# Kernel optimization log

Hardware: AMD Instinct MI355X
Metric: run time of the kernel (lower is better)

## Reference

```python
import jax, jax.numpy as jnp
import numpy as np

IN_DIM, HID, N_EXP, TOP_K = 4096, 512, 128, 2
SMOOTH = 0.1
SPARSITY = 0.5

def _gelu(x):
    return jax.nn.gelu(x, approximate=False)  # torch nn.GELU default (erf)


def setup_inputs() -> dict:
    key = jax.random.key(0)
    ks = jax.random.split(key, 24)
    def lin(k, fan_in, shape):
        bound = 1.0 / np.sqrt(fan_in)
        return jax.random.uniform(k, shape, jnp.float32, -bound, bound)
    x = jax.random.normal(ks[0], (4, 2048, IN_DIM), jnp.float32)
    # weights stored as (in, out); apply with x @ W + b
    w_in_proj = lin(ks[1], IN_DIM, (IN_DIM, HID)); b_in_proj = lin(ks[2], IN_DIM, (HID,))
    w_ff1 = lin(ks[3], 2 * HID, (2 * HID, HID)); b_ff1 = lin(ks[4], 2 * HID, (HID,))
    w_ff2 = lin(ks[5], HID, (HID, HID)); b_ff2 = lin(ks[6], HID, (HID,))
    w_ta = lin(ks[7], HID, (HID, HID)); b_ta = lin(ks[8], HID, (HID,))
    w_tb = lin(ks[9], HID, (HID, HID)); b_tb = lin(ks[10], HID, (HID,))
    w_iw = lin(ks[11], HID, (HID, HID)); b_iw = lin(ks[12], HID, (HID,))
    input_b = jnp.zeros((HID,), jnp.float32)
    mask = (jax.random.uniform(ks[13], (HID, HID)) > SPARSITY).astype(jnp.float32)
    w_rw = lin(ks[14], HID, (HID, HID)) * mask  # structured sparsity on recurrent weight
    r_b = jnp.zeros((HID,), jnp.float32)
    w_g1 = lin(ks[15], HID, (HID, 2 * HID)); b_g1 = lin(ks[16], HID, (2 * HID,))
    w_g2 = lin(ks[17], 2 * HID, (2 * HID, N_EXP)); b_g2 = lin(ks[18], 2 * HID, (N_EXP,))
    return dict(x=x, w_in_proj=w_in_proj, b_in_proj=b_in_proj, w_ff1=w_ff1, b_ff1=b_ff1,
                w_ff2=w_ff2, b_ff2=b_ff2, w_ta=w_ta, b_ta=b_ta, w_tb=w_tb, b_tb=b_tb,
                w_iw=w_iw, b_iw=b_iw, input_b=input_b, w_rw=w_rw, r_b=r_b,
                w_g1=w_g1, b_g1=b_g1, w_g2=w_g2, b_g2=b_g2)


def reference(x, w_in_proj, b_in_proj, w_ff1, b_ff1, w_ff2, b_ff2, w_ta, b_ta,
              w_tb, b_tb, w_iw, b_iw, input_b, w_rw, r_b, w_g1, b_g1, w_g2, b_g2):
    B, S, _ = x.shape
    ts = 1.0

    def step(carry, x_t):
        h, prev_probs, first = carry
        xt = x_t @ w_in_proj + b_in_proj                       # (B, HID)
        # CfC cell
        x_cat = jnp.concatenate([xt, h], axis=-1)
        ff1 = _gelu(x_cat @ w_ff1 + b_ff1)
        ff2 = _gelu(ff1 @ w_ff2 + b_ff2)
        t_a = ff2 @ w_ta + b_ta
        t_b = ff2 @ w_tb + b_tb
        t_interp = jax.nn.sigmoid(t_a * ts + t_b)
        inp_c = _gelu(xt @ w_iw + b_iw + input_b)
        rec_c = _gelu(h @ w_rw + r_b)
        new_h = h * (1.0 - t_interp) + t_interp * (inp_c + rec_c)
        # expert gate
        g = _gelu(new_h @ w_g1 + b_g1)
        probs = jax.nn.softmax(g @ w_g2 + b_g2, axis=-1)       # (B, N_EXP)
        probs = jnp.where(first, probs,
                          (1.0 - SMOOTH) * probs + SMOOTH * prev_probs)
        new_prev = jax.lax.stop_gradient(probs)                # .detach() in torch
        top_p, top_i = jax.lax.top_k(probs, TOP_K)
        top_w = top_p / jnp.sum(top_p, axis=-1, keepdims=True)
        return (new_h, new_prev, jnp.array(False)), (top_i, top_w)

    h0 = jnp.zeros((B, HID), x.dtype)
    p0 = jnp.zeros((B, N_EXP), x.dtype)
    carry0 = (h0, p0, jnp.array(True))
    _, (idx, wts) = jax.lax.scan(step, carry0, jnp.swapaxes(x, 0, 1))
    expert_indices = jnp.swapaxes(idx, 0, 1)   # (B, S, TOP_K)
    expert_weights = jnp.swapaxes(wts, 0, 1)   # (B, S, TOP_K)
    return expert_indices, expert_weights
```

## Files before the change

kernel.cpp:

```cpp
#include <hip/hip_runtime.h>
#include <cmath>

#define HID 512
#define NEXP 128
#define BB 4
#define SS 2048
#define NROW (BB*SS)
#define FAST_ITERS 96
#define FAIL_STICKY 12

typedef unsigned long long u64;
typedef unsigned int u32;

__device__ __forceinline__ float gelu_f(float x){
  return 0.5f*x*(1.0f + erff(x*0.70710678118654752440f));
}

__device__ __forceinline__ u64 aload64(const u64* p){
  return __hip_atomic_load(p, __ATOMIC_RELAXED, __HIP_MEMORY_SCOPE_AGENT);
}
__device__ __forceinline__ void astore64(u64* p, u64 v){
  __hip_atomic_store(p, v, __ATOMIC_RELAXED, __HIP_MEMORY_SCOPE_AGENT);
}
__device__ __forceinline__ void fstore64(u64* p, u64 v){
  asm volatile("global_store_dwordx2 %0, %1, off" :: "v"(p), "v"(v) : "memory");
}
__device__ __forceinline__ u64 packtag(float f, u32 tag){
  return ((u64)__float_as_uint(f) << 32) | (u64)tag;
}

__device__ __forceinline__ void poll2x(const u64* fb, const u64* mb, u32 tag,
                                       float* stg, int tid,
                                       int& fails, bool& use_agent){
  u64 v0 = 0, v1 = 0;
  bool ok0 = false, ok1 = false;
  if (!use_agent){
    const u64* p0 = fb + tid;
    const u64* p1 = fb + tid + 256;
    for (int it = 0; it < FAST_ITERS; ++it){
      u64 a, b;
      asm volatile("global_load_dwordx2 %0, %2, off sc0\n\t"
                   "global_load_dwordx2 %1, %3, off sc0\n\t"
                   "s_waitcnt vmcnt(0)"
                   : "=&v"(a), "=&v"(b) : "v"(p0), "v"(p1) : "memory");
      if (!ok0 && (u32)a == tag){ ok0 = true; v0 = a; }
      if (!ok1 && (u32)b == tag){ ok1 = true; v1 = b; }
      if (ok0 && ok1) break;
    }
    if (!(ok0 && ok1)){
      if (++fails >= FAIL_STICKY) use_agent = true;
    }
  }
  if (!ok0){ const u64* q = mb + tid;       u64 a; do { a = aload64(q); } while ((u32)a != tag); v0 = a; }
  if (!ok1){ const u64* q = mb + tid + 256; u64 a; do { a = aload64(q); } while ((u32)a != tag); v1 = a; }
  stg[tid]       = __uint_as_float((u32)(v0 >> 32));
  stg[tid + 256] = __uint_as_float((u32)(v1 >> 32));
}

__global__ __launch_bounds__(256) void biwc_k(const float* __restrict__ b_iw,
                                              const float* __restrict__ input_b,
                                              float* __restrict__ biwc)
{
  int i = blockIdx.x*256 + threadIdx.x;
  if (i < HID) biwc[i] = b_iw[i] + input_b[i];
}

template<bool GELU>
__global__ __launch_bounds__(256) void gemm_k(
    const float* __restrict__ A, const float* __restrict__ W,
    const float* __restrict__ bias, float* __restrict__ C,
    int M, int N, int K)
{
  __shared__ float As[16][68];
  __shared__ float Ws[16][68];
  const int tid = threadIdx.x;
  const int mb = blockIdx.y*64, nb = blockIdx.x*64;
  const int tx = tid & 15, ty = tid >> 4;
  const int am = tid >> 2, ak = (tid & 3)*4;
  const int wk = tid >> 4, wn = (tid & 15)*4;
  float acc[4][4] = {};
  const float* Aptr = A + (size_t)(mb+am)*K + ak;
  for (int kt = 0; kt < K; kt += 16){
    float4 av = *(const float4*)(Aptr + kt);
    float4 wv = *(const float4*)(W + (size_t)(kt+wk)*N + nb + wn);
    As[ak  ][am] = av.x; As[ak+1][am] = av.y; As[ak+2][am] = av.z; As[ak+3][am] = av.w;
    *(float4*)&Ws[wk][wn] = wv;
    __syncthreads();
#pragma unroll
    for (int kk = 0; kk < 16; kk++){
      float4 a4 = *(const float4*)&As[kk][ty*4];
      float4 w4 = *(const float4*)&Ws[kk][tx*4];
      float ar[4] = {a4.x, a4.y, a4.z, a4.w};
      float wr[4] = {w4.x, w4.y, w4.z, w4.w};
#pragma unroll
      for (int i = 0; i < 4; i++)
#pragma unroll
        for (int j = 0; j < 4; j++)
          acc[i][j] = fmaf(ar[i], wr[j], acc[i][j]);
    }
    __syncthreads();
  }
#pragma unroll
  for (int i = 0; i < 4; i++){
    int row = mb + ty*4 + i;
    float o[4];
#pragma unroll
    for (int j = 0; j < 4; j++){
      float v = acc[i][j] + bias[nb + tx*4 + j];
      o[j] = GELU ? gelu_f(v) : v;
    }
    float4 o4 = {o[0], o[1], o[2], o[3]};
    *(float4*)(C + (size_t)row*N + nb + tx*4) = o4;
  }
}

__global__ __launch_bounds__(256, 1) void scan_k(
    const float* __restrict__ w_ff1, const float* __restrict__ w_rw,
    const float* __restrict__ w_ff2,
    const float* __restrict__ w_ta, const float* __restrict__ w_tb,
    const float* __restrict__ bff2, const float* __restrict__ b_ta,
    const float* __restrict__ b_tb, const float* __restrict__ rb,
    const float* __restrict__ PRE, const float* __restrict__ INPC,
    float* __restrict__ Hout,
    u64* __restrict__ exh, u64* __restrict__ exf1, u64* __restrict__ exf2,
    u64* __restrict__ fexh, u64* __restrict__ fexf1, u64* __restrict__ fexf2)
{
  __shared__ float Wa2[512*32];
  __shared__ float Wb2[512*16];
  __shared__ float Wc2[512*16];
  __shared__ float stg[512];
  __shared__ float red[128];
  __shared__ float rec_loc[16];

  const int tid = threadIdx.x;
  const int b = blockIdx.x & 7;
  if (b >= BB) return;
  const int sub = blockIdx.x >> 3;
  const int col0 = sub*16;
  u64* exh_b   = exh   + b*512;
  u64* exf1_b  = exf1  + b*512;
  u64* exf2_b  = exf2  + b*512;
  u64* fexh_b  = fexh  + b*512;
  u64* fexf1_b = fexf1 + b*512;
  u64* fexf2_b = fexf2 + b*512;

  if (tid < 16) fstore64(&fexh_b[col0 + tid], packtag(0.f, 0u));

  for (int idx = tid; idx < 512*32; idx += 256){
    int k = idx >> 5, c = idx & 31;
    float v = (c < 16) ? w_ff1[(size_t)(512+k)*HID + col0 + c]
                       : w_rw[(size_t)k*HID + col0 + (c-16)];
    Wa2[((k>>1)<<6) + (c<<1) + (k&1)] = v;
  }
  for (int idx = tid; idx < 512*16; idx += 256){
    int k = idx >> 4, c = idx & 15;
    Wb2[((k>>1)<<5) + (c<<1) + (k&1)] = w_ff2[(size_t)k*HID + col0 + c];
    Wc2[((k>>1)<<5) + (c<<1) + (k&1)] = w_ta[(size_t)k*HID + col0 + c]
                                      + w_tb[(size_t)k*HID + col0 + c];
  }
  float b3v = 0.f, bff2v = 0.f, rbv = 0.f, h_reg = 0.f;
  if (tid < 16){ b3v = b_ta[col0+tid] + b_tb[col0+tid]; bff2v = bff2[col0+tid]; }
  if (tid >= 16 && tid < 32) rbv = rb[col0 + tid - 16];
  __syncthreads();

  const int cA = tid & 31, pA = tid >> 5;
  const int cB = tid & 15, pB = tid >> 4;
  int fails = 0; bool use_agent = false;

  for (int t = 0; t < SS; t++){
    float pre_v = 0.f, ic_v = 0.f;
    if (tid < 16){
      pre_v = PRE [((size_t)b*SS + t)*HID + col0 + tid];
      ic_v  = INPC[((size_t)b*SS + t)*HID + col0 + tid];
    }
    poll2x(fexh_b, exh_b, (u32)t, stg, tid, fails, use_agent);
    __syncthreads();
    {
      const float2* wp = (const float2*)(Wa2) + (pA<<5) + cA;
      const float2* hp = (const float2*)(stg) + pA;
      float a0=0.f, a1=0.f, a2=0.f, a3=0.f;
#pragma unroll
      for (int j = 0; j < 32; j += 2){
        float2 w0 = wp[(j+0)*256], h0 = hp[(j+0)*8];
        float2 w1 = wp[(j+1)*256], h1 = hp[(j+1)*8];
        a0 = fmaf(w0.x, h0.x, a0); a1 = fmaf(w0.y, h0.y, a1);
        a2 = fmaf(w1.x, h1.x, a2); a3 = fmaf(w1.y, h1.y, a3);
      }
      float acc = (a0+a1)+(a2+a3);
      acc += __shfl_xor(acc, 32);
      if ((tid & 32) == 0) red[(tid>>6)*32 + cA] = acc;
    }
    __syncthreads();
    if (tid < 32){
      float s = red[tid] + red[32+tid] + red[64+tid] + red[96+tid];
      if (tid < 16){
        float v = gelu_f(pre_v + s);
        u64 pk = packtag(v, (u32)(t+1));
        fstore64(&fexf1_b[col0 + tid], pk);
        astore64(&exf1_b[col0 + tid], pk);
      } else {
        rec_loc[tid-16] = gelu_f(s + rbv);
      }
    }
    poll2x(fexf1_b, exf1_b, (u32)(t+1), stg, tid, fails, use_agent);
    __syncthreads();
    {
      const float2* wp = (const float2*)(Wb2) + (pB<<4) + cB;
      const float2* hp = (const float2*)(stg) + pB;
      float a0=0.f, a1=0.f, a2=0.f, a3=0.f;
#pragma unroll
      for (int j = 0; j < 16; j += 2){
        float2 w0 = wp[(j+0)*256], h0 = hp[(j+0)*16];
        float2 w1 = wp[(j+1)*256], h1 = hp[(j+1)*16];
        a0 = fmaf(w0.x, h0.x, a0); a1 = fmaf(w0.y, h0.y, a1);
        a2 = fmaf(w1.x, h1.x, a2); a3 = fmaf(w1.y, h1.y, a3);
      }
      float acc = (a0+a1)+(a2+a3);
      acc += __shfl_xor(acc, 16);
      acc += __shfl_xor(acc, 32);
      if ((tid & 48) == 0) red[(tid>>6)*16 + cB] = acc;
    }
    __syncthreads();
    if (tid < 16){
      float s = red[tid] + red[16+tid] + red[32+tid] + red[48+tid];
      float v = gelu_f(s + bff2v);
      u64 pk = packtag(v, (u32)(t+1));
      fstore64(&fexf2_b[col0 + tid], pk);
      astore64(&exf2_b[col0 + tid], pk);
    }
    poll2x(fexf2_b, exf2_b, (u32)(t+1), stg, tid, fails, use_agent);
    __syncthreads();
    {
      const float2* wp = (const float2*)(Wc2) + (pB<<4) + cB;
      const float2* hp = (const float2*)(stg) + pB;
      float a0=0.f, a1=0.f, a2=0.f, a3=0.f;
#pragma unroll
      for (int j = 0; j < 16; j += 2){
        float2 w0 = wp[(j+0)*256], h0 = hp[(j+0)*16];
        float2 w1 = wp[(j+1)*256], h1 = hp[(j+1)*16];
        a0 = fmaf(w0.x, h0.x, a0); a1 = fmaf(w0.y, h0.y, a1);
        a2 = fmaf(w1.x, h1.x, a2); a3 = fmaf(w1.y, h1.y, a3);
      }
      float acc = (a0+a1)+(a2+a3);
      acc += __shfl_xor(acc, 16);
      acc += __shfl_xor(acc, 32);
      if ((tid & 48) == 0) red[(tid>>6)*16 + cB] = acc;
    }
    __syncthreads();
    if (tid < 16){
      float s = red[tid] + red[16+tid] + red[32+tid] + red[48+tid];
      float ti = 1.0f / (1.0f + expf(-(s + b3v)));
      float nh = h_reg*(1.0f - ti) + ti*(ic_v + rec_loc[tid]);
      h_reg = nh;
      u64 pk = packtag(nh, (u32)(t+1));
      fstore64(&fexh_b[col0 + tid], pk);
      astore64(&exh_b[col0 + tid], pk);
      Hout[((size_t)b*SS + t)*HID + col0 + tid] = nh;
    }
  }

  __syncthreads();
  for (int i = tid; i < 512; i += 256){
    fstore64(&fexh_b[i],  0xFFFFFFFFull);
    fstore64(&fexf1_b[i], 0xFFFFFFFFull);
    fstore64(&fexf2_b[i], 0xFFFFFFFFull);
  }
}

__global__ __launch_bounds__(256) void softmax_k(const float* __restrict__ LOGITS,
                                                 float* __restrict__ SM)
{
  int wv = threadIdx.x >> 6, lane = threadIdx.x & 63;
  int row = blockIdx.x*4 + wv;
  const float* xp = LOGITS + (size_t)row*NEXP;
  float x0 = xp[lane], x1 = xp[lane+64];
  float m = fmaxf(x0, x1);
#pragma unroll
  for (int d = 1; d < 64; d <<= 1) m = fmaxf(m, __shfl_xor(m, d));
  float e0 = expf(x0 - m), e1 = expf(x1 - m);
  float s = e0 + e1;
#pragma unroll
  for (int d = 1; d < 64; d <<= 1) s += __shfl_xor(s, d);
  float inv = 1.0f / s;
  float* op = SM + (size_t)row*NEXP;
  op[lane] = e0*inv; op[lane+64] = e1*inv;
}

__global__ __launch_bounds__(256) void smooth_topk_k(const float* __restrict__ SM,
                                                     float* __restrict__ out)
{
  int wv = threadIdx.x >> 6, lane = threadIdx.x & 63;
  int row = blockIdx.x*4 + wv;
  int b = row >> 11, t = row & 2047;
  const float* base = SM + (size_t)row*NEXP;
  float a0 = 0.f, a1 = 0.f;
  float coef = 0.9f;
  int nt = t < 20 ? t : 20;
  for (int j = 0; j < nt; j++){
    const float* pj = base - j*NEXP;
    a0 += coef * pj[lane];
    a1 += coef * pj[lane+64];
    coef *= 0.1f;
  }
  if (t < 20){
    const float* s0 = SM + (size_t)b*SS*NEXP;
    float c0 = coef * (1.0f/0.9f);
    a0 += c0 * s0[lane];
    a1 += c0 * s0[lane+64];
  }
  float v0, v1; int i0, i1;
  if (a0 >= a1){ v0=a0; i0=lane;    v1=a1; i1=lane+64; }
  else         { v0=a1; i0=lane+64; v1=a0; i1=lane;    }
#pragma unroll
  for (int d = 1; d < 64; d <<= 1){
    float ov0 = __shfl_xor(v0, d), ov1 = __shfl_xor(v1, d);
    int   oi0 = __shfl_xor(i0, d), oi1 = __shfl_xor(i1, d);
    bool firstMine = (v0 > ov0) || (v0 == ov0 && i0 < oi0);
    float nv0, nv1; int ni0, ni1;
    if (firstMine){
      nv0 = v0; ni0 = i0;
      bool s = (v1 > ov0) || (v1 == ov0 && i1 < oi0);
      nv1 = s ? v1 : ov0; ni1 = s ? i1 : oi0;
    } else {
      nv0 = ov0; ni0 = oi0;
      bool s = (ov1 > v0) || (ov1 == v0 && oi1 < i0);
      nv1 = s ? ov1 : v0; ni1 = s ? oi1 : i0;
    }
    v0 = nv0; v1 = nv1; i0 = ni0; i1 = ni1;
  }
  if (lane == 0){
    float ssum = v0 + v1;
    size_t o = (size_t)row*2;
    out[o]     = (float)i0;
    out[o+1]   = (float)i1;
    out[16384 + o]   = v0 / ssum;
    out[16384 + o+1] = v1 / ssum;
  }
}

extern "C" void kernel_launch(void* const* d_in, const int* in_sizes, int n_in,
                              void* d_out, int out_size, void* d_ws, size_t ws_size,
                              hipStream_t stream)
{
  (void)in_sizes; (void)n_in; (void)out_size;
  const float* x       = (const float*)d_in[0];
  const float* w_in    = (const float*)d_in[1];
  const float* b_in    = (const float*)d_in[2];
  const float* w_ff1   = (const float*)d_in[3];
  const float* b_ff1   = (const float*)d_in[4];
  const float* w_ff2   = (const float*)d_in[5];
  const float* b_ff2   = (const float*)d_in[6];
  const float* w_ta    = (const float*)d_in[7];
  const float* b_ta    = (const float*)d_in[8];
  const float* w_tb    = (const float*)d_in[9];
  const float* b_tb    = (const float*)d_in[10];
  const float* w_iw    = (const float*)d_in[11];
  const float* b_iw    = (const float*)d_in[12];
  const float* input_b = (const float*)d_in[13];
  const float* w_rw    = (const float*)d_in[14];
  const float* r_b     = (const float*)d_in[15];
  const float* w_g1    = (const float*)d_in[16];
  const float* b_g1    = (const float*)d_in[17];
  const float* w_g2    = (const float*)d_in[18];
  const float* b_g2    = (const float*)d_in[19];

  float* ws    = (float*)d_ws;
  float* XT    = ws + 0;
  float* PRE   = ws + 4194304;
  float* INPC  = ws + 8388608;
  float* Hbuf  = ws + 12582912;
  float* G1    = ws + 0;
  float* LOGB  = ws + 8388608;
  float* SM    = ws + 9437184;
  float* biwc  = ws + 16777216;
  u64*   exh   = (u64*)(ws + 16777728);
  u64*   exf1  = (u64*)(ws + 16781824);
  u64*   exf2  = (u64*)(ws + 16785920);
  u64*   fexh  = (u64*)(ws + 16790016);
  u64*   fexf1 = (u64*)(ws + 16794112);
  u64*   fexf2 = (u64*)(ws + 16798208);
  if (ws_size < (size_t)16802304 * sizeof(float)) return;

  hipMemsetAsync(ws + 16777728, 0, 3 * 2048 * sizeof(u64), stream);

  biwc_k<<<2, 256, 0, stream>>>(b_iw, input_b, biwc);
  gemm_k<false><<<dim3(8, 128), 256, 0, stream>>>(x, w_in, b_in, XT, NROW, 512, 4096);
  gemm_k<false><<<dim3(8, 128), 256, 0, stream>>>(XT, w_ff1, b_ff1, PRE, NROW, 512, 512);
  gemm_k<true ><<<dim3(8, 128), 256, 0, stream>>>(XT, w_iw, biwc, INPC, NROW, 512, 512);
  scan_k<<<256, 256, 0, stream>>>(w_ff1, w_rw, w_ff2, w_ta, w_tb,
                                  b_ff2, b_ta, b_tb, r_b,
                                  PRE, INPC, Hbuf, exh, exf1, exf2,
                                  fexh, fexf1, fexf2);
  gemm_k<true ><<<dim3(16, 128), 256, 0, stream>>>(Hbuf, w_g1, b_g1, G1, NROW, 1024, 512);
  gemm_k<false><<<dim3(2, 128), 256, 0, stream>>>(G1, w_g2, b_g2, LOGB, NROW, 128, 1024);
  softmax_k<<<2048, 256, 0, stream>>>(LOGB, SM);
  smooth_topk_k<<<2048, 256, 0, stream>>>(SM, (float*)d_out);
}
```

Measured before the change: 11.00 ms.

## Keep recurrent weights in registers and reduce via wave shuffles, drop block barriers

```diff
diff --git a/kernel.cpp b/kernel.cpp
--- a/kernel.cpp
+++ b/kernel.cpp
@@ -29,8 +29,8 @@
   return ((u64)__float_as_uint(f) << 32) | (u64)tag;
 }
 
-__device__ __forceinline__ void poll2x(const u64* fb, const u64* mb, u32 tag,
-                                       float* stg, int tid,
+__device__ __forceinline__ void poll2p(const u64* fb, const u64* mb, u32 tag,
+                                       float* stgp, int tid,
                                        int& fails, bool& use_agent){
   u64 v0 = 0, v1 = 0;
   bool ok0 = false, ok1 = false;
@@ -53,8 +53,9 @@
   }
   if (!ok0){ const u64* q = mb + tid;       u64 a; do { a = aload64(q); } while ((u32)a != tag); v0 = a; }
   if (!ok1){ const u64* q = mb + tid + 256; u64 a; do { a = aload64(q); } while ((u32)a != tag); v1 = a; }
-  stg[tid]       = __uint_as_float((u32)(v0 >> 32));
-  stg[tid + 256] = __uint_as_float((u32)(v1 >> 32));
+  int k0 = tid, k1 = tid + 256;
+  stgp[k0 + 4*(k0>>6)] = __uint_as_float((u32)(v0 >> 32));
+  stgp[k1 + 4*(k1>>6)] = __uint_as_float((u32)(v1 >> 32));
 }
 
 __global__ __launch_bounds__(256) void biwc_k(const float* __restrict__ b_iw,
@@ -125,11 +126,11 @@
     u64* __restrict__ exh, u64* __restrict__ exf1, u64* __restrict__ exf2,
     u64* __restrict__ fexh, u64* __restrict__ fexf1, u64* __restrict__ fexf2)
 {
-  __shared__ float Wa2[512*32];
-  __shared__ float Wb2[512*16];
-  __shared__ float Wc2[512*16];
-  __shared__ float stg[512];
-  __shared__ float red[128];
+  __shared__ float stg_h[544];
+  __shared__ float stg_f1[544];
+  __shared__ float stg_f2[544];
+  __shared__ float pre_buf[64*16];
+  __shared__ float ic_buf[64*16];
   __shared__ float rec_loc[16];
 
   const int tid = threadIdx.x;
@@ -144,121 +145,139 @@
   u64* fexf1_b = fexf1 + b*512;
   u64* fexf2_b = fexf2 + b*512;
 
-  if (tid < 16) fstore64(&fexh_b[col0 + tid], packtag(0.f, 0u));
-
-  for (int idx = tid; idx < 512*32; idx += 256){
-    int k = idx >> 5, c = idx & 31;
-    float v = (c < 16) ? w_ff1[(size_t)(512+k)*HID + col0 + c]
-                       : w_rw[(size_t)k*HID + col0 + (c-16)];
-    Wa2[((k>>1)<<6) + (c<<1) + (k&1)] = v;
-  }
-  for (int idx = tid; idx < 512*16; idx += 256){
-    int k = idx >> 4, c = idx & 15;
-    Wb2[((k>>1)<<5) + (c<<1) + (k&1)] = w_ff2[(size_t)k*HID + col0 + c];
-    Wc2[((k>>1)<<5) + (c<<1) + (k&1)] = w_ta[(size_t)k*HID + col0 + c]
-                                      + w_tb[(size_t)k*HID + col0 + c];
-  }
-  float b3v = 0.f, bff2v = 0.f, rbv = 0.f, h_reg = 0.f;
-  if (tid < 16){ b3v = b_ta[col0+tid] + b_tb[col0+tid]; bff2v = bff2[col0+tid]; }
-  if (tid >= 16 && tid < 32) rbv = rb[col0 + tid - 16];
-  __syncthreads();
-
-  const int cA = tid & 31, pA = tid >> 5;
-  const int cB = tid & 15, pB = tid >> 4;
+  const int w = tid >> 6, l = tid & 63;
+  const int outA = w*8 + (l & 7), kpA = l >> 3;
+  const int outB = w*4 + (l & 3), kpB = l >> 2;
+
+  if (l < 4) fstore64(&fexh_b[col0 + outB], packtag(0.f, 0u));
+
+  float wA[64], wB[32], wC[32];
+  {
+    const float* srcA = (outA < 16)
+        ? (w_ff1 + (size_t)(512 + kpA*64)*HID + col0 + outA)
+        : (w_rw  + (size_t)(kpA*64)*HID + col0 + outA - 16);
+#pragma unroll
+    for (int j = 0; j < 64; j++) wA[j] = srcA[(size_t)j*HID];
+    const float* srcB  = w_ff2 + (size_t)(kpB*32)*HID + col0 + outB;
+    const float* srcC1 = w_ta  + (size_t)(kpB*32)*HID + col0 + outB;
+    const float* srcC2 = w_tb  + (size_t)(kpB*32)*HID + col0 + outB;
+#pragma unroll
+    for (int j = 0; j < 32; j++){
+      wB[j] = srcB[(size_t)j*HID];
+      wC[j] = srcC1[(size_t)j*HID] + srcC2[(size_t)j*HID];
+    }
+  }
+  const float rbv   = (outA >= 16) ? rb[col0 + outA - 16] : 0.f;
+  const float bff2v = bff2[col0 + outB];
+  const float b3v   = b_ta[col0 + outB] + b_tb[col0 + outB];
+  float h_reg = 0.f;
+
+  const int baseA = kpA*68;
+  const int baseB = kpB*32 + 4*(kpB >> 1);
+
   int fails = 0; bool use_agent = false;
 
   for (int t = 0; t < SS; t++){
-    float pre_v = 0.f, ic_v = 0.f;
-    if (tid < 16){
-      pre_v = PRE [((size_t)b*SS + t)*HID + col0 + tid];
-      ic_v  = INPC[((size_t)b*SS + t)*HID + col0 + tid];
-    }
-    poll2x(fexh_b, exh_b, (u32)t, stg, tid, fails, use_agent);
+    if ((t & 63) == 0){
+      __syncthreads();
+      int s = tid >> 2, j4 = (tid & 3) << 2;
+      float4 pv = *(const float4*)(PRE  + ((size_t)b*SS + t + s)*HID + col0 + j4);
+      float4 qv = *(const float4*)(INPC + ((size_t)b*SS + t + s)*HID + col0 + j4);
+      *(float4*)&pre_buf[s*16 + j4] = pv;
+      *(float4*)&ic_buf [s*16 + j4] = qv;
+    }
+    poll2p(fexh_b, exh_b, (u32)t, stg_h, tid, fails, use_agent);
     __syncthreads();
     {
-      const float2* wp = (const float2*)(Wa2) + (pA<<5) + cA;
-      const float2* hp = (const float2*)(stg) + pA;
+      const float* hp = &stg_h[baseA];
       float a0=0.f, a1=0.f, a2=0.f, a3=0.f;
 #pragma unroll
-      for (int j = 0; j < 32; j += 2){
-        float2 w0 = wp[(j+0)*256], h0 = hp[(j+0)*8];
-        float2 w1 = wp[(j+1)*256], h1 = hp[(j+1)*8];
-        a0 = fmaf(w0.x, h0.x, a0); a1 = fmaf(w0.y, h0.y, a1);
-        a2 = fmaf(w1.x, h1.x, a2); a3 = fmaf(w1.y, h1.y, a3);
+      for (int j = 0; j < 16; j++){
+        float4 h4 = *(const float4*)(hp + j*4);
+        a0 = fmaf(h4.x, wA[j*4+0], a0);
+        a1 = fmaf(h4.y, wA[j*4+1], a1);
+        a2 = fmaf(h4.z, wA[j*4+2], a2);
+        a3 = fmaf(h4.w, wA[j*4+3], a3);
       }
       float acc = (a0+a1)+(a2+a3);
+      acc += __shfl_xor(acc, 8);
+      acc += __shfl_xor(acc, 16);
       acc += __shfl_xor(acc, 32);
-      if ((tid & 32) == 0) red[(tid>>6)*32 + cA] = acc;
-    }
-    __syncthreads();
-    if (tid < 32){
-      float s = red[tid] + red[32+tid] + red[64+tid] + red[96+tid];
-      if (tid < 16){
-        float v = gelu_f(pre_v + s);
-        u64 pk = packtag(v, (u32)(t+1));
-        fstore64(&fexf1_b[col0 + tid], pk);
-        astore64(&exf1_b[col0 + tid], pk);
-      } else {
-        rec_loc[tid-16] = gelu_f(s + rbv);
-      }
-    }
-    poll2x(fexf1_b, exf1_b, (u32)(t+1), stg, tid, fails, use_agent);
+      if (l < 8){
+        if (outA < 16){
+          float v = gelu_f(pre_buf[(t & 63)*16 + outA] + acc);
+          u64 pk = packtag(v, (u32)(t+1));
+          fstore64(&fexf1_b[col0 + outA], pk);
+          astore64(&exf1_b[col0 + outA], pk);
+        } else {
+          rec_loc[outA - 16] = gelu_f(acc + rbv);
+        }
+      }
+    }
+    poll2p(fexf1_b, exf1_b, (u32)(t+1), stg_f1, tid, fails, use_agent);
     __syncthreads();
     {
-      const float2* wp = (const float2*)(Wb2) + (pB<<4) + cB;
-      const float2* hp = (const float2*)(stg) + pB;
+      const float* fp = &stg_f1[baseB];
       float a0=0.f, a1=0.f, a2=0.f, a3=0.f;
 #pragma unroll
-      for (int j = 0; j < 16; j += 2){
-        float2 w0 = wp[(j+0)*256], h0 = hp[(j+0)*16];
-        float2 w1 = wp[(j+1)*256], h1 = hp[(j+1)*16];
-        a0 = fmaf(w0.x, h0.x, a0); a1 = fmaf(w0.y, h0.y, a1);
-        a2 = fmaf(w1.x, h1.x, a2); a3 = fmaf(w1.y, h1.y, a3);
+      for (int j = 0; j < 8; j++){
+        float4 f4 = *(const float4*)(fp + j*4);
+        a0 = fmaf(f4.x, wB[j*4+0], a0);
+        a1 = fmaf(f4.y, wB[j*4+1], a1);
+        a2 = fmaf(f4.z, wB[j*4+2], a2);
+        a3 = fmaf(f4.w, wB[j*4+3], a3);
       }
       float acc = (a0+a1)+(a2+a3);
+      acc += __shfl_xor(acc, 4);
+      acc += __shfl_xor(acc, 8);
       acc += __shfl_xor(acc, 16);
       acc += __shfl_xor(acc, 32);
-      if ((tid & 48) == 0) red[(tid>>6)*16 + cB] = acc;
-    }
-    __syncthreads();
-    if (tid < 16){
-      float s = red[tid] + red[16+tid] + red[32+tid] + red[48+tid];
-      float v = gelu_f(s + bff2v);
-      u64 pk = packtag(v, (u32)(t+1));
-      fstore64(&fexf2_b[col0 + tid], pk);
-      astore64(&exf2_b[col0 + tid], pk);
-    }
-    poll2x(fexf2_b, exf2_b, (u32)(t+1), stg, tid, fails, use_agent);
+      if (l < 4){
+        float v = gelu_f(acc + bff2v);
+        u64 pk = packtag(v, (u32)(t+1));
+        fstore64(&fexf2_b[col0 + outB], pk);
+        astore64(&exf2_b[col0 + outB], pk);
+      }
+    }
+    poll2p(fexf2_b, exf2_b, (u32)(t+1), stg_f2, tid, fails, use_agent);
     __syncthreads();
     {
-      const float2* wp = (const float2*)(Wc2) + (pB<<4) + cB;
-      const float2* hp = (const float2*)(stg) + pB;
+      const float* fp = &stg_f2[baseB];
       float a0=0.f, a1=0.f, a2=0.f, a3=0.f;
 #pragma unroll
-      for (int j = 0; j < 16; j += 2){
-        float2 w0 = wp[(j+0)*256], h0 = hp[(j+0)*16];
-        float2 w1 = wp[(j+1)*256], h1 = hp[(j+1)*16];
-        a0 = fmaf(w0.x, h0.x, a0); a1 = fmaf(w0.y, h0.y, a1);
-        a2 = fmaf(w1.x, h1.x, a2); a3 = fmaf(w1.y, h1.y, a3);
+      for (int j = 0; j < 8; j++){
+        float4 f4 = *(const float4*)(fp + j*4);
+        a0 = fmaf(f4.x, wC[j*4+0], a0);
+        a1 = fmaf(f4.y, wC[j*4+1], a1);
+        a2 = fmaf(f4.z, wC[j*4+2], a2);
+        a3 = fmaf(f4.w, wC[j*4+3], a3);
       }
       float acc = (a0+a1)+(a2+a3);
+      acc += __shfl_xor(acc, 4);
+      acc += __shfl_xor(acc, 8);
       acc += __shfl_xor(acc, 16);
       acc += __shfl_xor(acc, 32);
-      if ((tid & 48) == 0) red[(tid>>6)*16 + cB] = acc;
-    }
-    __syncthreads();
-    if (tid < 16){
-      float s = red[tid] + red[16+tid] + red[32+tid] + red[48+tid];
-      float ti = 1.0f / (1.0f + expf(-(s + b3v)));
-      float nh = h_reg*(1.0f - ti) + ti*(ic_v + rec_loc[tid]);
+      float ti = 1.0f / (1.0f + expf(-(acc + b3v)));
+      float rc = rec_loc[outB];
+      float ic = ic_buf[(t & 63)*16 + outB];
+      float nh = h_reg*(1.0f - ti) + ti*(ic + rc);
       h_reg = nh;
-      u64 pk = packtag(nh, (u32)(t+1));
-      fstore64(&fexh_b[col0 + tid], pk);
-      astore64(&exh_b[col0 + tid], pk);
-      Hout[((size_t)b*SS + t)*HID + col0 + tid] = nh;
-    }
-  }
-
+      if (l < 4){
+        u64 pk = packtag(nh, (u32)(t+1));
+        fstore64(&fexh_b[col0 + outB], pk);
+        astore64(&exh_b[col0 + outB], pk);
+        Hout[((size_t)b*SS + t)*HID + col0 + outB] = nh;
+      }
+    }
+  }
+
+  {
+    const u64* q0 = exh_b + tid;
+    const u64* q1 = exh_b + tid + 256;
+    u64 a;
+    do { a = aload64(q0); } while ((u32)a != (u32)SS);
+    do { a = aload64(q1); } while ((u32)a != (u32)SS);
+  }
   __syncthreads();
   for (int i = tid; i < 512; i += 256){
     fstore64(&fexh_b[i],  0xFFFFFFFFull);
```

New measurement: 13.67 ms. 24.3% more time.

## Bind scan chains to XCDs via hardware XCC ID and dynamic slot claiming

Applied to the files above, without the earlier changes.

```diff
diff --git a/kernel.cpp b/kernel.cpp
--- a/kernel.cpp
+++ b/kernel.cpp
@@ -7,7 +7,8 @@
 #define SS 2048
 #define NROW (BB*SS)
 #define FAST_ITERS 96
-#define FAIL_STICKY 12
+#define FAIL_STICKY 16
+#define WARMUP_T 16
 
 typedef unsigned long long u64;
 typedef unsigned int u32;
@@ -22,6 +23,9 @@
 __device__ __forceinline__ void astore64(u64* p, u64 v){
   __hip_atomic_store(p, v, __ATOMIC_RELAXED, __HIP_MEMORY_SCOPE_AGENT);
 }
+__device__ __forceinline__ int aloadi(const int* p){
+  return __hip_atomic_load(p, __ATOMIC_RELAXED, __HIP_MEMORY_SCOPE_AGENT);
+}
 __device__ __forceinline__ void fstore64(u64* p, u64 v){
   asm volatile("global_store_dwordx2 %0, %1, off" :: "v"(p), "v"(v) : "memory");
 }
@@ -31,7 +35,7 @@
 
 __device__ __forceinline__ void poll2x(const u64* fb, const u64* mb, u32 tag,
                                        float* stg, int tid,
-                                       int& fails, bool& use_agent){
+                                       int& fails, bool& use_agent, bool count){
   u64 v0 = 0, v1 = 0;
   bool ok0 = false, ok1 = false;
   if (!use_agent){
@@ -47,7 +51,7 @@
       if (!ok1 && (u32)b == tag){ ok1 = true; v1 = b; }
       if (ok0 && ok1) break;
     }
-    if (!(ok0 && ok1)){
+    if (!(ok0 && ok1) && count){
       if (++fails >= FAIL_STICKY) use_agent = true;
     }
   }
@@ -123,7 +127,8 @@
     const float* __restrict__ PRE, const float* __restrict__ INPC,
     float* __restrict__ Hout,
     u64* __restrict__ exh, u64* __restrict__ exf1, u64* __restrict__ exf2,
-    u64* __restrict__ fexh, u64* __restrict__ fexf1, u64* __restrict__ fexf2)
+    u64* __restrict__ fexh, u64* __restrict__ fexf1, u64* __restrict__ fexf2,
+    int* __restrict__ ctl)
 {
   __shared__ float Wa2[512*32];
   __shared__ float Wb2[512*16];
@@ -131,12 +136,40 @@
   __shared__ float stg[512];
   __shared__ float red[128];
   __shared__ float rec_loc[16];
+  __shared__ int sh_chain, sh_sub;
 
   const int tid = threadIdx.x;
-  const int b = blockIdx.x & 7;
-  if (b >= BB) return;
-  const int sub = blockIdx.x >> 3;
+
+  if (tid == 0){
+    u32 xcc;
+    asm volatile("s_getreg_b32 %0, hwreg(HW_REG_XCC_ID)" : "=s"(xcc));
+    int xcd = (int)(xcc & 7);
+    int chain = -1, sub = -1;
+    if (xcd < BB){
+      int s = __hip_atomic_fetch_add(&ctl[xcd], 1, __ATOMIC_RELAXED, __HIP_MEMORY_SCOPE_AGENT);
+      if (s < 32){ chain = xcd; sub = s;
+        __hip_atomic_fetch_add(&ctl[4], 1, __ATOMIC_RELAXED, __HIP_MEMORY_SCOPE_AGENT); }
+    }
+    if (chain < 0){
+      for (int spin = 0; spin < 8000; ++spin){
+        if (aloadi(&ctl[4]) >= BB*32) break;
+        __builtin_amdgcn_s_sleep(2);
+      }
+      if (aloadi(&ctl[4]) < BB*32){
+        for (int c = 0; c < BB && chain < 0; c++){
+          int s = __hip_atomic_fetch_add(&ctl[c], 1, __ATOMIC_RELAXED, __HIP_MEMORY_SCOPE_AGENT);
+          if (s < 32){ chain = c; sub = s;
+            __hip_atomic_fetch_add(&ctl[4], 1, __ATOMIC_RELAXED, __HIP_MEMORY_SCOPE_AGENT); }
+        }
+      }
+    }
+    sh_chain = chain; sh_sub = sub;
+  }
+  __syncthreads();
+  const int b = sh_chain, sub = sh_sub;
+  if (b < 0) return;
   const int col0 = sub*16;
+
   u64* exh_b   = exh   + b*512;
   u64* exf1_b  = exf1  + b*512;
   u64* exf2_b  = exf2  + b*512;
@@ -163,17 +196,25 @@
   if (tid >= 16 && tid < 32) rbv = rb[col0 + tid - 16];
   __syncthreads();
 
+  if (tid == 0){
+    __hip_atomic_fetch_add(&ctl[8 + b], 1, __ATOMIC_RELEASE, __HIP_MEMORY_SCOPE_AGENT);
+    while (__hip_atomic_load(&ctl[8 + b], __ATOMIC_ACQUIRE, __HIP_MEMORY_SCOPE_AGENT) < 32)
+      __builtin_amdgcn_s_sleep(1);
+  }
+  __syncthreads();
+
   const int cA = tid & 31, pA = tid >> 5;
   const int cB = tid & 15, pB = tid >> 4;
   int fails = 0; bool use_agent = false;
 
   for (int t = 0; t < SS; t++){
+    const bool count = (t >= WARMUP_T);
     float pre_v = 0.f, ic_v = 0.f;
     if (tid < 16){
       pre_v = PRE [((size_t)b*SS + t)*HID + col0 + tid];
       ic_v  = INPC[((size_t)b*SS + t)*HID + col0 + tid];
     }
-    poll2x(fexh_b, exh_b, (u32)t, stg, tid, fails, use_agent);
+    poll2x(fexh_b, exh_b, (u32)t, stg, tid, fails, use_agent, count);
     __syncthreads();
     {
       const float2* wp = (const float2*)(Wa2) + (pA<<5) + cA;
@@ -202,7 +243,7 @@
         rec_loc[tid-16] = gelu_f(s + rbv);
       }
     }
-    poll2x(fexf1_b, exf1_b, (u32)(t+1), stg, tid, fails, use_agent);
+    poll2x(fexf1_b, exf1_b, (u32)(t+1), stg, tid, fails, use_agent, count);
     __syncthreads();
     {
       const float2* wp = (const float2*)(Wb2) + (pB<<4) + cB;
@@ -228,7 +269,7 @@
       fstore64(&fexf2_b[col0 + tid], pk);
       astore64(&exf2_b[col0 + tid], pk);
     }
-    poll2x(fexf2_b, exf2_b, (u32)(t+1), stg, tid, fails, use_agent);
+    poll2x(fexf2_b, exf2_b, (u32)(t+1), stg, tid, fails, use_agent, count);
     __syncthreads();
     {
       const float2* wp = (const float2*)(Wc2) + (pB<<4) + cB;
@@ -259,6 +300,13 @@
     }
   }
 
+  {
+    const u64* q0 = exh_b + tid;
+    const u64* q1 = exh_b + tid + 256;
+    u64 a;
+    do { a = aload64(q0); } while ((u32)a != (u32)SS);
+    do { a = aload64(q1); } while ((u32)a != (u32)SS);
+  }
   __syncthreads();
   for (int i = tid; i < 512; i += 256){
     fstore64(&fexh_b[i],  0xFFFFFFFFull);
@@ -379,18 +427,20 @@
   u64*   fexh  = (u64*)(ws + 16790016);
   u64*   fexf1 = (u64*)(ws + 16794112);
   u64*   fexf2 = (u64*)(ws + 16798208);
-  if (ws_size < (size_t)16802304 * sizeof(float)) return;
+  int*   ctl   = (int*)(ws + 16802304);
+  if (ws_size < (size_t)16802368 * sizeof(float)) return;
 
   hipMemsetAsync(ws + 16777728, 0, 3 * 2048 * sizeof(u64), stream);
+  hipMemsetAsync(ctl, 0, 16 * sizeof(int), stream);
 
   biwc_k<<<2, 256, 0, stream>>>(b_iw, input_b, biwc);
   gemm_k<false><<<dim3(8, 128), 256, 0, stream>>>(x, w_in, b_in, XT, NROW, 512, 4096);
   gemm_k<false><<<dim3(8, 128), 256, 0, stream>>>(XT, w_ff1, b_ff1, PRE, NROW, 512, 512);
   gemm_k<true ><<<dim3(8, 128), 256, 0, stream>>>(XT, w_iw, biwc, INPC, NROW, 512, 512);
-  scan_k<<<256, 256, 0, stream>>>(w_ff1, w_rw, w_ff2, w_ta, w_tb,
-                                  b_ff2, b_ta, b_tb, r_b,
-                                  PRE, INPC, Hbuf, exh, exf1, exf2,
-                                  fexh, fexf1, fexf2);
+  scan_k<<<2048, 256, 0, stream>>>(w_ff1, w_rw, w_ff2, w_ta, w_tb,
+                                   b_ff2, b_ta, b_tb, r_b,
+                                   PRE, INPC, Hbuf, exh, exf1, exf2,
+                                   fexh, fexf1, fexf2, ctl);
   gemm_k<true ><<<dim3(16, 128), 256, 0, stream>>>(Hbuf, w_g1, b_g1, G1, NROW, 1024, 512);
   gemm_k<false><<<dim3(2, 128), 256, 0, stream>>>(G1, w_g2, b_g2, LOGB, NROW, 128, 1024);
   softmax_k<<<2048, 256, 0, stream>>>(LOGB, SM);
```

Measured after the change: 11.61 ms. +5.6%, slower.
